# Performance work log

Hardware: AMD Instinct MI355X
Metric: run time of the kernel (lower is better)

Reference implementation:

```python
import jax, jax.numpy as jnp
import numpy as np

DIM = 1024
HEADS = 16


def setup_inputs() -> dict:
    key = jax.random.key(0)
    k1, k2, k3, k4 = jax.random.split(key, 4)
    x = jax.random.normal(k1, (4, 2048, DIM), dtype=jnp.float32)
    s = 1.0 / np.sqrt(DIM)
    w_qkv = jax.random.normal(k2, (DIM, 3 * DIM), dtype=jnp.float32) * s
    w_out = jax.random.normal(k3, (DIM, DIM), dtype=jnp.float32) * s
    b_out = jax.random.normal(k4, (DIM,), dtype=jnp.float32) * 0.01
    return {"x": x, "w_qkv": w_qkv, "w_out": w_out, "b_out": b_out}


def reference(x, w_qkv, w_out, b_out):
    b, n, d = x.shape
    h = HEADS
    dh = d // h
    scale = dh ** -0.5
    qkv = x @ w_qkv  # [b, n, 3d]
    q, k, v = jnp.split(qkv, 3, axis=-1)
    # [b, n, d] -> [b, h, n, dh]
    def to_heads(t):
        return t.reshape(b, n, h, dh).transpose(0, 2, 1, 3)
    q, k, v = to_heads(q), to_heads(k), to_heads(v)
    dots = jnp.einsum('bhid,bhjd->bhij', q, k) * scale
    attn = jax.nn.softmax(dots, axis=-1)
    out = jnp.einsum('bhij,bhjd->bhid', attn, v)
    out = out.transpose(0, 2, 1, 3).reshape(b, n, d)
    return out @ w_out + b_out
```

## Files before the change

### kernel.cpp

```cpp
#include <hip/hip_runtime.h>
#include <hip/hip_bf16.h>


typedef __attribute__((ext_vector_type(4))) float f32x4;
typedef __attribute__((ext_vector_type(16))) float f32x16;
typedef __attribute__((ext_vector_type(8))) unsigned short u16x8;
typedef __attribute__((ext_vector_type(4))) unsigned short u16x4;
typedef __attribute__((ext_vector_type(4))) unsigned int u32x4;
typedef __attribute__((ext_vector_type(8))) __bf16 bf16x8;

static __device__ __forceinline__ f32x4 mfma_bf16(u16x8 a, u16x8 b, f32x4 c) {
    return __builtin_amdgcn_mfma_f32_16x16x32_bf16(
        __builtin_bit_cast(bf16x8, a), __builtin_bit_cast(bf16x8, b), c, 0, 0, 0);
}
static __device__ __forceinline__ f32x16 mfma32(u16x8 a, u16x8 b, f32x16 c) {
    return __builtin_amdgcn_mfma_f32_32x32x16_bf16(
        __builtin_bit_cast(bf16x8, a), __builtin_bit_cast(bf16x8, b), c, 0, 0, 0);
}

static __device__ __forceinline__ unsigned short f2bf(float f) {
    unsigned int u = __builtin_bit_cast(unsigned int, f);
    u += 0x7fffu + ((u >> 16) & 1u);
    return (unsigned short)(u >> 16);
}
static __device__ __forceinline__ unsigned int cvt_pk_bf16(float a, float b) {
    unsigned int r;
    asm("v_cvt_pk_bf16_f32 %0, %1, %2" : "=v"(r) : "v"(a), "v"(b));
    return r;
}
static __device__ __forceinline__ float fexp2(float x) {
    float r;
    asm("v_exp_f32 %0, %1" : "=v"(r) : "v"(x));
    return r;
}
static __device__ __forceinline__ float frcp(float x) {
    float r;
    asm("v_rcp_f32 %0, %1" : "=v"(r) : "v"(x));
    return r;
}
typedef const __attribute__((address_space(1))) unsigned int* gp1_t;
typedef __attribute__((address_space(3))) unsigned int* lp3_t;
static __device__ __forceinline__ void gl_lds16(const void* g, void* l) {
    __builtin_amdgcn_global_load_lds((gp1_t)g, (lp3_t)l, 16, 0, 0);
}

__global__ void k_cvt(const float* __restrict__ in, unsigned short* __restrict__ out, int n4) {
    int i = blockIdx.x * blockDim.x + threadIdx.x;
    int stride = gridDim.x * blockDim.x;
    for (; i < n4; i += stride) {
        f32x4 v = ((const f32x4*)in)[i];
        u16x4 o;
        #pragma unroll
        for (int j = 0; j < 4; ++j) o[j] = f2bf(v[j]);
        ((u16x4*)out)[i] = o;
    }
}

__global__ void k_transpose(const float* __restrict__ in, unsigned short* __restrict__ out,
                            int R, int C) {
    __shared__ float tile[32][33];
    int c0 = blockIdx.x * 32, r0 = blockIdx.y * 32;
    int tx = threadIdx.x, ty = threadIdx.y;
    #pragma unroll
    for (int i = ty; i < 32; i += 8)
        tile[i][tx] = in[(size_t)(r0 + i) * C + c0 + tx];
    __syncthreads();
    #pragma unroll
    for (int i = ty; i < 32; i += 8)
        out[(size_t)(c0 + i) * R + r0 + tx] = f2bf(tile[tx][i]);
}

__global__ __launch_bounds__(256, 4) void k_gemm1(
    const unsigned short* __restrict__ A,
    const unsigned short* __restrict__ BT,
    unsigned short* __restrict__ Qs,
    unsigned short* __restrict__ Ks,
    unsigned short* __restrict__ VTs)
{
    __shared__ unsigned short As[2][128 * 32];
    __shared__ unsigned short Bs[2][128 * 32];
    const int K = 1024;
    const int tid = threadIdx.x, lane = tid & 63, wave = tid >> 6;

    int lin = blockIdx.y * 24 + blockIdx.x;
    int xcd = lin & 7, idx = lin >> 3;
    int virt = xcd * 192 + idx;
    int bx = virt >> 6, by = virt & 63;
    const int m0 = by * 128, n0 = bx * 128;

    const int wm = (wave >> 1) * 64, wn = (wave & 1) * 64;
    const int lr = lane & 15, half = lane >> 4;

    const int srow_in = lane >> 2, sslot = lane & 3;
    auto stage = [&](int buf, int t) {
        int k0 = t * 32;
        #pragma unroll
        for (int c = 0; c < 2; ++c) {
            int chunk = wave * 2 + c;
            int row = chunk * 16 + srow_in;
            int gk = (sslot ^ ((row >> 1) & 3)) * 8;
            gl_lds16(&A[(size_t)(m0 + row) * K + k0 + gk], &As[buf][chunk * 512]);
            gl_lds16(&BT[(size_t)(n0 + row) * K + k0 + gk], &Bs[buf][chunk * 512]);
        }
    };

    f32x4 acc[4][4] = {};

    stage(0, 0);
    __syncthreads();

    for (int t = 0; t < 32; ++t) {
        const int cur = t & 1;
        if (t < 31) stage(cur ^ 1, t + 1);
        const unsigned short* Ab = As[cur];
        const unsigned short* Bb = Bs[cur];

        u16x8 af[4], bfr[4];
        #pragma unroll
        for (int i = 0; i < 4; ++i) {
            int ra = wm + i * 16 + lr;
            af[i] = *(const u16x8*)&Ab[ra * 32 + ((half ^ ((ra >> 1) & 3)) * 8)];
            int rb = wn + i * 16 + lr;
            bfr[i] = *(const u16x8*)&Bb[rb * 32 + ((half ^ ((rb >> 1) & 3)) * 8)];
        }
        __builtin_amdgcn_s_setprio(1);
        #pragma unroll
        for (int i = 0; i < 4; ++i)
            #pragma unroll
            for (int j = 0; j < 4; ++j)
                acc[i][j] = mfma_bf16(af[i], bfr[j], acc[i][j]);
        __builtin_amdgcn_s_setprio(0);

        __syncthreads();
    }

    #pragma unroll
    for (int i = 0; i < 4; ++i) {
        int rowb = m0 + wm + i * 16 + half * 4;
        int b = rowb >> 11, n = rowb & 2047;
        int bh16 = (b << 4);
        #pragma unroll
        for (int j = 0; j < 4; ++j) {
            int col = n0 + wn + j * 16 + lr;
            int part = col >> 10, cj = col & 1023;
            int h = cj >> 6, d = cj & 63;
            int bh = bh16 + h;
            if (part == 0) {
                #pragma unroll
                for (int r = 0; r < 4; ++r)
                    Qs[((size_t)bh * 2048 + n + r) * 64 + d] = f2bf(acc[i][j][r] * 0.18033688f);
            } else if (part == 1) {
                #pragma unroll
                for (int r = 0; r < 4; ++r)
                    Ks[((size_t)bh * 2048 + n + r) * 64 + d] = f2bf(acc[i][j][r]);
            } else {
                u16x4 p;
                #pragma unroll
                for (int r = 0; r < 4; ++r) p[r] = f2bf(acc[i][j][r]);
                *(u16x4*)&VTs[((size_t)bh * 64 + d) * 2048 + n] = p;
            }
        }
    }
}

__global__ __launch_bounds__(512, 1) void k_gemm2(
    const unsigned short* __restrict__ A,
    const unsigned short* __restrict__ BT,
    const float* __restrict__ bias,
    float* __restrict__ outf)
{
    __shared__ unsigned short As[3][256 * 64];
    __shared__ unsigned short Bs[3][128 * 64];
    const int K = 1024;
    const int tid = threadIdx.x, lane = tid & 63, wave = tid >> 6;

    int gx = gridDim.x;
    int nwg = gx * gridDim.y;
    int lin = blockIdx.y * gx + blockIdx.x;
    int virt = (lin & 7) * (nwg >> 3) + (lin >> 3);
    int bx = virt % gx, by = virt / gx;
    const int m0 = by * 256, n0 = bx * 128;

    const int wm = (wave >> 1) * 64, wn = (wave & 1) * 64;
    const int lr = lane & 15, half = lane >> 4;
    const int srow = lane >> 3, sslot = lane & 7;

    auto stage_sub = [&](int buf, int t, int h) {
        int k0 = t * 64;
        #pragma unroll
        for (int r = 0; r < 2; ++r) {
            int chunk = (h * 2 + r) * 8 + wave;
            int row = chunk * 8 + srow;
            int koff = (sslot ^ (row & 7)) * 8;
            gl_lds16(&A[(size_t)(m0 + row) * K + k0 + koff], &As[buf][chunk * 512]);
        }
        {
            int chunk = h * 8 + wave;
            int row = chunk * 8 + srow;
            int koff = (sslot ^ (row & 7)) * 8;
            gl_lds16(&BT[(size_t)(n0 + row) * K + k0 + koff], &Bs[buf][chunk * 512]);
        }
    };

    f32x4 acc[4][4] = {};

    stage_sub(0, 0, 0); stage_sub(0, 0, 1);
    stage_sub(1, 1, 0); stage_sub(1, 1, 1);
    asm volatile("s_waitcnt vmcnt(6)" ::: "memory");
    __builtin_amdgcn_s_barrier();

    for (int t = 0; t < 16; ++t) {
        const int cur = t % 3, nxt = (t + 2) % 3;
        const bool do_stage = (t + 2) < 16;
        const unsigned short* Ab = As[cur];
        const unsigned short* Bb = Bs[cur];

        #pragma unroll
        for (int ks = 0; ks < 2; ++ks) {
            u16x8 af[4], bfr[4];
            #pragma unroll
            for (int i = 0; i < 4; ++i) {
                int ra = wm + i * 16 + lr;
                af[i] = *(const u16x8*)&Ab[ra * 64 + (((ks * 4 + half) ^ (ra & 7)) * 8)];
                int rb = wn + i * 16 + lr;
                bfr[i] = *(const u16x8*)&Bb[rb * 64 + (((ks * 4 + half) ^ (rb & 7)) * 8)];
            }
            if (do_stage) stage_sub(nxt, t + 2, ks);
            if (ks == 1) {
                if (t < 14)       asm volatile("s_waitcnt vmcnt(6)" ::: "memory");
                else if (t == 14) asm volatile("s_waitcnt vmcnt(0)" ::: "memory");
            }
            __builtin_amdgcn_s_barrier();
            asm volatile("s_waitcnt lgkmcnt(0)" ::: "memory");
            __builtin_amdgcn_sched_barrier(0);
            __builtin_amdgcn_s_setprio(1);
            #pragma unroll
            for (int i = 0; i < 4; ++i)
                #pragma unroll
                for (int j = 0; j < 4; ++j)
                    acc[i][j] = mfma_bf16(af[i], bfr[j], acc[i][j]);
            __builtin_amdgcn_s_setprio(0);
            __builtin_amdgcn_s_barrier();
        }
    }

    #pragma unroll
    for (int i = 0; i < 4; ++i)
        #pragma unroll
        for (int j = 0; j < 4; ++j)
            #pragma unroll
            for (int r = 0; r < 4; ++r) {
                int row = m0 + wm + i * 16 + half * 4 + r;
                int col = n0 + wn + j * 16 + lr;
                outf[(size_t)row * 1024 + col] = acc[i][j][r] + bias[col];
            }
}

__global__ __launch_bounds__(256, 4) void k_attn(
    const unsigned short* __restrict__ Qs,
    const unsigned short* __restrict__ Ks,
    const unsigned short* __restrict__ VTs,
    unsigned short* __restrict__ attn)
{
    __shared__ unsigned short Kt[2][64 * 64];
    __shared__ unsigned short Vt[2][64 * 64];
    const int tid = threadIdx.x, lane = tid & 63, wave = tid >> 6;

    int lin = blockIdx.y * 16 + blockIdx.x;
    int virt = (lin & 7) * 128 + (lin >> 3);
    int bh = virt >> 4;
    int q0 = (virt & 15) * 128 + wave * 32;

    const int lq = lane & 31;
    const int hi = lane >> 5;
    const bool hib = hi != 0;

    const unsigned short* Kbase = Ks + (size_t)bh * 2048 * 64;
    const unsigned short* Vbase = VTs + (size_t)bh * 64 * 2048;

    u16x8 qf[4];
    {
        const unsigned short* Qr = Qs + ((size_t)bh * 2048 + q0 + lq) * 64;
        #pragma unroll
        for (int kk = 0; kk < 4; ++kk)
            qf[kk] = *(const u16x8*)&Qr[kk * 16 + hi * 8];
    }

    const int srow_in = lane >> 4, sslot = lane & 15;
    auto stage = [&](int buf, int j0) {
        #pragma unroll
        for (int c = 0; c < 2; ++c) {
            int chunk = wave * 2 + c;
            int row = chunk * 4 + srow_in;
            int v = sslot ^ (row & 15);
            int high = v >> 3, dsl = (v & 7) * 8;
            gl_lds16(Kbase + (size_t)(j0 + high * 32 + row) * 64 + dsl, &Kt[buf][chunk * 512]);
            gl_lds16(Vbase + (size_t)(high * 32 + row) * 2048 + j0 + dsl, &Vt[buf][chunk * 512]);
        }
    };

    f32x16 o[2] = {};
    f32x16 osum = {};
    const u16x8 onesf = {0x3F80, 0x3F80, 0x3F80, 0x3F80, 0x3F80, 0x3F80, 0x3F80, 0x3F80};

    stage(0, 0);
    __syncthreads();
    int cur = 0;

    for (int t = 0; t < 32; ++t) {
        if (t < 31) stage(cur ^ 1, (t + 1) * 64);

        f32x16 sacc[2] = {};
        __builtin_amdgcn_s_setprio(1);
        #pragma unroll
        for (int jb = 0; jb < 2; ++jb) {
            u16x8 kf[4];
            #pragma unroll
            for (int kk = 0; kk < 4; ++kk) {
                int s = (jb * 8 + kk * 2 + hi) ^ (lq & 15);
                kf[kk] = *(const u16x8*)&Kt[cur][lq * 128 + s * 8];
            }
            #pragma unroll
            for (int kk = 0; kk < 4; ++kk)
                sacc[jb] = mfma32(kf[kk], qf[kk], sacc[jb]);
        }
        __builtin_amdgcn_s_setprio(0);

        unsigned int pk[16];
        #pragma unroll
        for (int jb = 0; jb < 2; ++jb)
            #pragma unroll
            for (int i = 0; i < 8; ++i)
                pk[jb * 8 + i] = cvt_pk_bf16(fexp2(sacc[jb][2 * i]), fexp2(sacc[jb][2 * i + 1]));

        #pragma unroll
        for (int kk = 0; kk < 4; ++kk) {
            const int base = (kk >> 1) * 8 + (kk & 1) * 4;
            unsigned int a0 = pk[base + 0], a1 = pk[base + 1], a2 = pk[base + 2], a3 = pk[base + 3];
            unsigned int sa0 = __shfl_xor(a0, 32), sa1 = __shfl_xor(a1, 32);
            unsigned int sa2 = __shfl_xor(a2, 32), sa3 = __shfl_xor(a3, 32);
            u32x4 w0;
            w0[0] = hib ? sa2 : a0;  w0[1] = hib ? sa3 : a1;
            w0[2] = hib ? a2 : sa0;  w0[3] = hib ? a3 : sa1;
            u16x8 pa = __builtin_bit_cast(u16x8, w0);
            __builtin_amdgcn_s_setprio(1);
            osum = mfma32(pa, onesf, osum);
            #pragma unroll
            for (int db = 0; db < 2; ++db) {
                int s = (db * 8 + kk * 2 + hi) ^ (lq & 15);
                u16x8 vf = *(const u16x8*)&Vt[cur][lq * 128 + s * 8];
                o[db] = mfma32(pa, vf, o[db]);
            }
            __builtin_amdgcn_s_setprio(0);
        }

        __syncthreads();
        cur ^= 1;
    }

    int b = bh >> 4, h = bh & 15;
    #pragma unroll
    for (int r = 0; r < 16; ++r) {
        int qrow = (r & 3) + 8 * (r >> 2) + 4 * hi;
        float invr = frcp(osum[r]);
        size_t ro = (size_t)(b * 2048 + q0 + qrow) * 1024 + h * 64;
        attn[ro + lq]      = f2bf(o[0][r] * invr);
        attn[ro + 32 + lq] = f2bf(o[1][r] * invr);
    }
}

extern "C" void kernel_launch(void* const* d_in, const int* in_sizes, int n_in,
                              void* d_out, int out_size, void* d_ws, size_t ws_size,
                              hipStream_t stream) {
    const float* x     = (const float*)d_in[0];
    const float* w_qkv = (const float*)d_in[1];
    const float* w_out = (const float*)d_in[2];
    const float* b_out = (const float*)d_in[3];
    float* out = (float*)d_out;

    char* ws = (char*)d_ws;
    size_t off = 0;
    auto alloc = [&](size_t bytes) -> void* {
        void* p = ws + off;
        off += (bytes + 255) & ~(size_t)255;
        return p;
    };
    unsigned short* xb    = (unsigned short*)alloc(8192ull * 1024 * 2);
    unsigned short* wqkvT = (unsigned short*)alloc(3072ull * 1024 * 2);
    unsigned short* woutT = (unsigned short*)alloc(1024ull * 1024 * 2);
    unsigned short* Qs    = (unsigned short*)alloc(64ull * 2048 * 64 * 2);
    unsigned short* Ks    = (unsigned short*)alloc(64ull * 2048 * 64 * 2);
    unsigned short* VTs   = (unsigned short*)alloc(64ull * 2048 * 64 * 2);
    unsigned short* attn  = (unsigned short*)alloc(8192ull * 1024 * 2);
    if (off > ws_size) return;

    k_cvt<<<2048, 256, 0, stream>>>(x, xb, 8192 * 1024 / 4);
    k_transpose<<<dim3(3072 / 32, 1024 / 32), dim3(32, 8), 0, stream>>>(w_qkv, wqkvT, 1024, 3072);
    k_transpose<<<dim3(1024 / 32, 1024 / 32), dim3(32, 8), 0, stream>>>(w_out, woutT, 1024, 1024);
    k_gemm1<<<dim3(24, 64), 256, 0, stream>>>(xb, wqkvT, Qs, Ks, VTs);
    k_attn<<<dim3(16, 64), 256, 0, stream>>>(Qs, Ks, VTs, attn);
    k_gemm2<<<dim3(8, 32), 512, 0, stream>>>(attn, woutT, b_out, out);
}
```

Before: 208.4 us.

## Rework QKV GEMM to 256x128 triple-buffered tiles with row-major output

The QKV projection GEMM now uses 512-thread blocks with 256x128 tiles, a K-step of 64 and a three-stage LDS pipeline with explicit waitcnt and barriers, matching the output GEMM's structure. It writes a plain row-major bf16 qkv buffer instead of scattered per-head Q/K/V^T stores. The Q scale is folded into the weight transpose, and a separate small kernel transposes V. Attention reads Q and K directly from the strided qkv buffer, and the attention output reuses the xb buffer. This trades the scattered epilogue stores for an extra V transpose pass and strided K loads in attention.

```diff
diff --git a/kernel.cpp b/kernel.cpp
--- a/kernel.cpp
+++ b/kernel.cpp
@@ -56,8 +56,8 @@
     }
 }
 
-__global__ void k_transpose(const float* __restrict__ in, unsigned short* __restrict__ out,
-                            int R, int C) {
+__global__ void k_transpose_sc(const float* __restrict__ in, unsigned short* __restrict__ out,
+                               int R, int C, int scale_rows, float scale) {
     __shared__ float tile[32][33];
     int c0 = blockIdx.x * 32, r0 = blockIdx.y * 32;
     int tx = threadIdx.x, ty = threadIdx.y;
@@ -66,101 +66,119 @@
         tile[i][tx] = in[(size_t)(r0 + i) * C + c0 + tx];
     __syncthreads();
     #pragma unroll
-    for (int i = ty; i < 32; i += 8)
-        out[(size_t)(c0 + i) * R + r0 + tx] = f2bf(tile[tx][i]);
-}
-
-__global__ __launch_bounds__(256, 4) void k_gemm1(
+    for (int i = ty; i < 32; i += 8) {
+        float v = tile[tx][i];
+        if (c0 + i < scale_rows) v *= scale;
+        out[(size_t)(c0 + i) * R + r0 + tx] = f2bf(v);
+    }
+}
+
+__global__ __launch_bounds__(512, 1) void k_gemm1(
     const unsigned short* __restrict__ A,
     const unsigned short* __restrict__ BT,
-    unsigned short* __restrict__ Qs,
-    unsigned short* __restrict__ Ks,
-    unsigned short* __restrict__ VTs)
+    unsigned short* __restrict__ qkv)
 {
-    __shared__ unsigned short As[2][128 * 32];
-    __shared__ unsigned short Bs[2][128 * 32];
+    __shared__ unsigned short As[3][256 * 64];
+    __shared__ unsigned short Bs[3][128 * 64];
     const int K = 1024;
     const int tid = threadIdx.x, lane = tid & 63, wave = tid >> 6;
 
     int lin = blockIdx.y * 24 + blockIdx.x;
     int xcd = lin & 7, idx = lin >> 3;
-    int virt = xcd * 192 + idx;
-    int bx = virt >> 6, by = virt & 63;
-    const int m0 = by * 128, n0 = bx * 128;
+    int virt = xcd * 96 + idx;
+    int by = virt / 24, bx = virt % 24;
+    const int m0 = by * 256, n0 = bx * 128;
 
     const int wm = (wave >> 1) * 64, wn = (wave & 1) * 64;
     const int lr = lane & 15, half = lane >> 4;
-
-    const int srow_in = lane >> 2, sslot = lane & 3;
-    auto stage = [&](int buf, int t) {
-        int k0 = t * 32;
-        #pragma unroll
-        for (int c = 0; c < 2; ++c) {
-            int chunk = wave * 2 + c;
-            int row = chunk * 16 + srow_in;
-            int gk = (sslot ^ ((row >> 1) & 3)) * 8;
-            gl_lds16(&A[(size_t)(m0 + row) * K + k0 + gk], &As[buf][chunk * 512]);
-            gl_lds16(&BT[(size_t)(n0 + row) * K + k0 + gk], &Bs[buf][chunk * 512]);
+    const int srow = lane >> 3, sslot = lane & 7;
+
+    auto stage_sub = [&](int buf, int t, int h) {
+        int k0 = t * 64;
+        #pragma unroll
+        for (int r = 0; r < 2; ++r) {
+            int chunk = (h * 2 + r) * 8 + wave;
+            int row = chunk * 8 + srow;
+            int koff = (sslot ^ (row & 7)) * 8;
+            gl_lds16(&A[(size_t)(m0 + row) * K + k0 + koff], &As[buf][chunk * 512]);
+        }
+        {
+            int chunk = h * 8 + wave;
+            int row = chunk * 8 + srow;
+            int koff = (sslot ^ (row & 7)) * 8;
+            gl_lds16(&BT[(size_t)(n0 + row) * K + k0 + koff], &Bs[buf][chunk * 512]);
         }
     };
 
     f32x4 acc[4][4] = {};
 
-    stage(0, 0);
-    __syncthreads();
-
-    for (int t = 0; t < 32; ++t) {
-        const int cur = t & 1;
-        if (t < 31) stage(cur ^ 1, t + 1);
+    stage_sub(0, 0, 0); stage_sub(0, 0, 1);
+    stage_sub(1, 1, 0); stage_sub(1, 1, 1);
+    asm volatile("s_waitcnt vmcnt(6)" ::: "memory");
+    __builtin_amdgcn_s_barrier();
+
+    for (int t = 0; t < 16; ++t) {
+        const int cur = t % 3, nxt = (t + 2) % 3;
+        const bool do_stage = (t + 2) < 16;
         const unsigned short* Ab = As[cur];
         const unsigned short* Bb = Bs[cur];
 
-        u16x8 af[4], bfr[4];
-        #pragma unroll
-        for (int i = 0; i < 4; ++i) {
-            int ra = wm + i * 16 + lr;
-            af[i] = *(const u16x8*)&Ab[ra * 32 + ((half ^ ((ra >> 1) & 3)) * 8)];
-            int rb = wn + i * 16 + lr;
-            bfr[i] = *(const u16x8*)&Bb[rb * 32 + ((half ^ ((rb >> 1) & 3)) * 8)];
-        }
-        __builtin_amdgcn_s_setprio(1);
-        #pragma unroll
-        for (int i = 0; i < 4; ++i)
-            #pragma unroll
-            for (int j = 0; j < 4; ++j)
-                acc[i][j] = mfma_bf16(af[i], bfr[j], acc[i][j]);
-        __builtin_amdgcn_s_setprio(0);
-
-        __syncthreads();
-    }
-
-    #pragma unroll
-    for (int i = 0; i < 4; ++i) {
-        int rowb = m0 + wm + i * 16 + half * 4;
-        int b = rowb >> 11, n = rowb & 2047;
-        int bh16 = (b << 4);
-        #pragma unroll
-        for (int j = 0; j < 4; ++j) {
-            int col = n0 + wn + j * 16 + lr;
-            int part = col >> 10, cj = col & 1023;
-            int h = cj >> 6, d = cj & 63;
-            int bh = bh16 + h;
-            if (part == 0) {
+        #pragma unroll
+        for (int ks = 0; ks < 2; ++ks) {
+            u16x8 af[4], bfr[4];
+            #pragma unroll
+            for (int i = 0; i < 4; ++i) {
+                int ra = wm + i * 16 + lr;
+                af[i] = *(const u16x8*)&Ab[ra * 64 + (((ks * 4 + half) ^ (ra & 7)) * 8)];
+                int rb = wn + i * 16 + lr;
+                bfr[i] = *(const u16x8*)&Bb[rb * 64 + (((ks * 4 + half) ^ (rb & 7)) * 8)];
+            }
+            if (do_stage) stage_sub(nxt, t + 2, ks);
+            if (ks == 1) {
+                if (t < 14)       asm volatile("s_waitcnt vmcnt(6)" ::: "memory");
+                else if (t == 14) asm volatile("s_waitcnt vmcnt(0)" ::: "memory");
+            }
+            __builtin_amdgcn_s_barrier();
+            asm volatile("s_waitcnt lgkmcnt(0)" ::: "memory");
+            __builtin_amdgcn_sched_barrier(0);
+            __builtin_amdgcn_s_setprio(1);
+            #pragma unroll
+            for (int i = 0; i < 4; ++i)
                 #pragma unroll
-                for (int r = 0; r < 4; ++r)
-                    Qs[((size_t)bh * 2048 + n + r) * 64 + d] = f2bf(acc[i][j][r] * 0.18033688f);
-            } else if (part == 1) {
-                #pragma unroll
-                for (int r = 0; r < 4; ++r)
-                    Ks[((size_t)bh * 2048 + n + r) * 64 + d] = f2bf(acc[i][j][r]);
-            } else {
-                u16x4 p;
-                #pragma unroll
-                for (int r = 0; r < 4; ++r) p[r] = f2bf(acc[i][j][r]);
-                *(u16x4*)&VTs[((size_t)bh * 64 + d) * 2048 + n] = p;
-            }
-        }
-    }
+                for (int j = 0; j < 4; ++j)
+                    acc[i][j] = mfma_bf16(af[i], bfr[j], acc[i][j]);
+            __builtin_amdgcn_s_setprio(0);
+            __builtin_amdgcn_s_barrier();
+        }
+    }
+
+    #pragma unroll
+    for (int i = 0; i < 4; ++i)
+        #pragma unroll
+        for (int j = 0; j < 4; ++j)
+            #pragma unroll
+            for (int r = 0; r < 4; ++r) {
+                int row = m0 + wm + i * 16 + half * 4 + r;
+                int col = n0 + wn + j * 16 + lr;
+                qkv[(size_t)row * 3072 + col] = f2bf(acc[i][j][r]);
+            }
+}
+
+__global__ void k_vtrans(const unsigned short* __restrict__ qkv,
+                         unsigned short* __restrict__ VTs) {
+    __shared__ unsigned short tile[32][33];
+    int bh = blockIdx.y >> 1, dt = blockIdx.y & 1;
+    int b = bh >> 4, h = bh & 15;
+    int n0 = blockIdx.x * 32, d0 = dt * 32;
+    int tx = threadIdx.x, ty = threadIdx.y;
+    const unsigned short* src = qkv + (size_t)(b * 2048) * 3072 + 2048 + h * 64 + d0;
+    #pragma unroll
+    for (int i = ty; i < 32; i += 8)
+        tile[i][tx] = src[(size_t)(n0 + i) * 3072 + tx];
+    __syncthreads();
+    #pragma unroll
+    for (int i = ty; i < 32; i += 8)
+        VTs[((size_t)bh * 64 + d0 + i) * 2048 + n0 + tx] = tile[tx][i];
 }
 
 __global__ __launch_bounds__(512, 1) void k_gemm2(
@@ -257,8 +275,7 @@
 }
 
 __global__ __launch_bounds__(256, 4) void k_attn(
-    const unsigned short* __restrict__ Qs,
-    const unsigned short* __restrict__ Ks,
+    const unsigned short* __restrict__ qkv,
     const unsigned short* __restrict__ VTs,
     unsigned short* __restrict__ attn)
 {
@@ -275,12 +292,13 @@
     const int hi = lane >> 5;
     const bool hib = hi != 0;
 
-    const unsigned short* Kbase = Ks + (size_t)bh * 2048 * 64;
+    int b = bh >> 4, h = bh & 15;
+    const unsigned short* Kq = qkv + (size_t)(b * 2048) * 3072 + 1024 + h * 64;
     const unsigned short* Vbase = VTs + (size_t)bh * 64 * 2048;
 
     u16x8 qf[4];
     {
-        const unsigned short* Qr = Qs + ((size_t)bh * 2048 + q0 + lq) * 64;
+        const unsigned short* Qr = qkv + (size_t)(b * 2048 + q0 + lq) * 3072 + h * 64;
         #pragma unroll
         for (int kk = 0; kk < 4; ++kk)
             qf[kk] = *(const u16x8*)&Qr[kk * 16 + hi * 8];
@@ -294,7 +312,7 @@
             int row = chunk * 4 + srow_in;
             int v = sslot ^ (row & 15);
             int high = v >> 3, dsl = (v & 7) * 8;
-            gl_lds16(Kbase + (size_t)(j0 + high * 32 + row) * 64 + dsl, &Kt[buf][chunk * 512]);
+            gl_lds16(Kq + (size_t)(j0 + high * 32 + row) * 3072 + dsl, &Kt[buf][chunk * 512]);
             gl_lds16(Vbase + (size_t)(high * 32 + row) * 2048 + j0 + dsl, &Vt[buf][chunk * 512]);
         }
     };
@@ -358,7 +376,6 @@
         cur ^= 1;
     }
 
-    int b = bh >> 4, h = bh & 15;
     #pragma unroll
     for (int r = 0; r < 16; ++r) {
         int qrow = (r & 3) + 8 * (r >> 2) + 4 * hi;
@@ -388,16 +405,17 @@
     unsigned short* xb    = (unsigned short*)alloc(8192ull * 1024 * 2);
     unsigned short* wqkvT = (unsigned short*)alloc(3072ull * 1024 * 2);
     unsigned short* woutT = (unsigned short*)alloc(1024ull * 1024 * 2);
-    unsigned short* Qs    = (unsigned short*)alloc(64ull * 2048 * 64 * 2);
-    unsigned short* Ks    = (unsigned short*)alloc(64ull * 2048 * 64 * 2);
+    unsigned short* qkv   = (unsigned short*)alloc(8192ull * 3072 * 2);
     unsigned short* VTs   = (unsigned short*)alloc(64ull * 2048 * 64 * 2);
-    unsigned short* attn  = (unsigned short*)alloc(8192ull * 1024 * 2);
     if (off > ws_size) return;
 
     k_cvt<<<2048, 256, 0, stream>>>(x, xb, 8192 * 1024 / 4);
-    k_transpose<<<dim3(3072 / 32, 1024 / 32), dim3(32, 8), 0, stream>>>(w_qkv, wqkvT, 1024, 3072);
-    k_transpose<<<dim3(1024 / 32, 1024 / 32), dim3(32, 8), 0, stream>>>(w_out, woutT, 1024, 1024);
-    k_gemm1<<<dim3(24, 64), 256, 0, stream>>>(xb, wqkvT, Qs, Ks, VTs);
-    k_attn<<<dim3(16, 64), 256, 0, stream>>>(Qs, Ks, VTs, attn);
-    k_gemm2<<<dim3(8, 32), 512, 0, stream>>>(attn, woutT, b_out, out);
-}
+    k_transpose_sc<<<dim3(3072 / 32, 1024 / 32), dim3(32, 8), 0, stream>>>(
+        w_qkv, wqkvT, 1024, 3072, 1024, 0.18033688f);
+    k_transpose_sc<<<dim3(1024 / 32, 1024 / 32), dim3(32, 8), 0, stream>>>(
+        w_out, woutT, 1024, 1024, 0, 1.0f);
+    k_gemm1<<<dim3(24, 32), 512, 0, stream>>>(xb, wqkvT, qkv);
+    k_vtrans<<<dim3(64, 128), dim3(32, 8), 0, stream>>>(qkv, VTs);
+    k_attn<<<dim3(16, 64), 256, 0, stream>>>(qkv, VTs, xb);
+    k_gemm2<<<dim3(8, 32), 512, 0, stream>>>(xb, woutT, b_out, out);
+}
```

Measured after the change: 203.6 us. 2.3% less time.
